# Optimization experiments

Hardware: AMD Instinct MI355X
Metric: run time of the kernel (lower is better)

The kernel has to match this reference:

```python
import jax, jax.numpy as jnp
import numpy as np

DY = jnp.array([-1, -1, -1, 0, 0, 0, 1, 1, 1], dtype=jnp.float32)
DX = jnp.array([-1, 0, 1, -1, 0, 1, -1, 0, 1], dtype=jnp.float32)
REG = jnp.stack([DY, DX])  # (2,9) regular_matrix: row0 = dy, row1 = dx
EPS = 1e-5


def conv3x3(x, w, b):
    y = jax.lax.conv_general_dilated(x, w, (1, 1), ((1, 1), (1, 1)),
                                     dimension_numbers=('NCHW', 'OIHW', 'NCHW'))
    return y + b[None, :, None, None]


def batchnorm(x, gamma, beta):
    m = x.mean((0, 2, 3), keepdims=True)
    v = x.var((0, 2, 3), keepdims=True)
    return gamma[None, :, None, None] * (x - m) * jax.lax.rsqrt(v + EPS) + beta[None, :, None, None]


def make_offset(tm, tr):
    # tm: (N,4,H,W) per-pixel 2x2 matrix, tr: (N,2,H,W) translation
    N, _, H, W = tm.shape
    M = tm.transpose(0, 2, 3, 1).reshape(N, H, W, 2, 2)
    off = jnp.einsum('nhwij,jk->nhwik', M, REG) - REG          # (N,H,W,2,9)
    off = off.transpose(0, 4, 3, 1, 2)                          # (N,9,2,H,W)
    off = off + tr[:, None, :, :, :]                            # broadcast translation over K
    return off


def deform_conv(x, off, w):
    # x: (N,C,H,W), off: (N,9,2,H,W) with [...,0]=dy,[...,1]=dx, w: (Co,C,3,3)
    N, C, H, W = x.shape
    K = 9
    py = jnp.arange(H, dtype=x.dtype)[None, None, :, None] + DY[None, :, None, None] + off[:, :, 0]
    px = jnp.arange(W, dtype=x.dtype)[None, None, None, :] + DX[None, :, None, None] + off[:, :, 1]
    y0 = jnp.floor(py)
    x0 = jnp.floor(px)
    wy = py - y0
    wx = px - x0
    y0i = y0.astype(jnp.int32)
    x0i = x0.astype(jnp.int32)
    x_flat = x.reshape(N, C, H * W)

    def corner(yi, xi, wgt):
        valid = (yi >= 0) & (yi < H) & (xi >= 0) & (xi < W)
        idx = jnp.clip(yi, 0, H - 1) * W + jnp.clip(xi, 0, W - 1)   # (N,K,H,W)
        g = jax.vmap(lambda xf, ix: xf[:, ix])(x_flat, idx.reshape(N, -1))
        g = g.reshape(N, C, K, H, W)
        return g * (wgt * valid)[:, None]

    cols = (corner(y0i, x0i, (1 - wy) * (1 - wx))
            + corner(y0i, x0i + 1, (1 - wy) * wx)
            + corner(y0i + 1, x0i, wy * (1 - wx))
            + corner(y0i + 1, x0i + 1, wy * wx))
    Co = w.shape[0]
    return jnp.einsum('nckhw,ock->nohw', cols, w.reshape(Co, C, K))


def setup_inputs() -> dict:
    key = jax.random.key(0)
    ks = jax.random.split(key, 16)
    N, C, Co, H, W = 4, 256, 256, 64, 64
    s_off = 0.02   # small init so offsets stay near the regular grid
    s_w = 0.05
    return {
        'x': jax.random.normal(ks[0], (N, C, H, W), jnp.float32),
        'tm1_w': jax.random.normal(ks[1], (4, C, 3, 3), jnp.float32) * s_off,
        'tm1_b': jax.random.normal(ks[2], (4,), jnp.float32) * s_off,
        'tr1_w': jax.random.normal(ks[3], (2, C, 3, 3), jnp.float32) * s_off,
        'tr1_b': jax.random.normal(ks[4], (2,), jnp.float32) * s_off,
        'dcn1_w': jax.random.normal(ks[5], (Co, C, 3, 3), jnp.float32) * s_w,
        'bn1_g': jnp.ones((Co,), jnp.float32),
        'bn1_b': jnp.zeros((Co,), jnp.float32),
        'tm2_w': jax.random.normal(ks[6], (4, Co, 3, 3), jnp.float32) * s_off,
        'tm2_b': jax.random.normal(ks[7], (4,), jnp.float32) * s_off,
        'tr2_w': jax.random.normal(ks[8], (2, Co, 3, 3), jnp.float32) * s_off,
        'tr2_b': jax.random.normal(ks[9], (2,), jnp.float32) * s_off,
        'dcn2_w': jax.random.normal(ks[10], (Co, Co, 3, 3), jnp.float32) * s_w,
        'bn2_g': jnp.ones((Co,), jnp.float32),
        'bn2_b': jnp.zeros((Co,), jnp.float32),
    }


def reference(x, tm1_w, tm1_b, tr1_w, tr1_b, dcn1_w, bn1_g, bn1_b,
              tm2_w, tm2_b, tr2_w, tr2_b, dcn2_w, bn2_g, bn2_b):
    residual = x
    off1 = make_offset(conv3x3(x, tm1_w, tm1_b), conv3x3(x, tr1_w, tr1_b))
    out = deform_conv(x, off1, dcn1_w)
    out = jax.nn.relu(batchnorm(out, bn1_g, bn1_b))
    off2 = make_offset(conv3x3(out, tm2_w, tm2_b), conv3x3(out, tr2_w, tr2_b))
    out = deform_conv(out, off2, dcn2_w)
    out = batchnorm(out, bn2_g, bn2_b)
    return jax.nn.relu(out + residual)
```

## Files before the change

### kernel.cpp

```cpp
#include <hip/hip_runtime.h>
#include <hip/hip_bf16.h>

#define HH 64
#define WW 64
#define HWSZ 4096
#define NBATCH 4
#define CCH 256
#define NPIX 16384
#define CK 2304
#define EPSB 1e-5f

typedef __attribute__((ext_vector_type(8))) short bf16x8;
typedef __attribute__((ext_vector_type(4))) float f32x4;

static __device__ __forceinline__ unsigned short f2bf(float f){
  __hip_bfloat16 h = __float2bfloat16(f);
  return *(unsigned short*)&h;
}

#if __has_builtin(__builtin_amdgcn_global_load_lds)
#define GLD(S,D) __builtin_amdgcn_global_load_lds((const __attribute__((address_space(1))) void*)(S), \
                                                  (__attribute__((address_space(3))) void*)(D), 16, 0, 0)
#else
#define GLD(S,D) (*(bf16x8*)((char*)(D) + lane*16) = *(const bf16x8*)(S))
#endif

__global__ __launch_bounds__(256) void k_transpose_in(const float* __restrict__ x,
                                                      float* __restrict__ xT){
  __shared__ float tile[64][65];
  int hw0 = blockIdx.x * 64;
  int c0  = blockIdx.y * 64;
  int n   = blockIdx.z;
  int t = threadIdx.x;
  int col = t & 63, rb = t >> 6;
#pragma unroll
  for (int r = 0; r < 16; ++r){
    int cl = rb + r*4;
    tile[cl][col] = x[(size_t)(n*CCH + c0 + cl)*HWSZ + hw0 + col];
  }
  __syncthreads();
#pragma unroll
  for (int r = 0; r < 16; ++r){
    int hwl = rb + r*4;
    xT[(size_t)(n*HWSZ + hw0 + hwl)*CCH + c0 + col] = tile[col][hwl];
  }
}

__global__ void k_woff_perm(const float* __restrict__ tmw, const float* __restrict__ trw,
                            float* __restrict__ woff){
  int idx = blockIdx.x*256 + threadIdx.x;
  if (idx >= 9*6*CCH) return;
  int k = idx / (6*CCH); int rem = idx % (6*CCH); int j = rem >> 8; int c = rem & 255;
  float v = (j < 4) ? tmw[(size_t)(j*CCH + c)*9 + k]
                    : trw[(size_t)((j-4)*CCH + c)*9 + k];
  woff[idx] = v;
}

__global__ void k_wgemm_perm(const float* __restrict__ w, __hip_bfloat16* __restrict__ wp){
  int idx = blockIdx.x*256 + threadIdx.x;
  if (idx >= CCH*CK) return;
  int blk = idx >> 13;
  int e   = idx & 8191;
  int o   = e >> 5;
  int el  = e & 31;
  int tap = blk >> 3, cb = blk & 7;
  int c   = cb*32 + (el ^ ((o & 3) << 3));
  wp[idx] = __float2bfloat16(w[(size_t)o*CK + c*9 + tap]);
}

__global__ __launch_bounds__(256) void k_offsets(const float* __restrict__ src,
    const float* __restrict__ wofft, const float* __restrict__ tmb,
    const float* __restrict__ trb, float* __restrict__ off){
  int t = threadIdx.x;
  int wid = t >> 6, lane = t & 63;
  int pbase = blockIdx.x*32 + wid*8;
  int n = pbase >> 12; int hw = pbase & 4095; int h = hw >> 6; int w0 = hw & 63;
  const float* base = src + (size_t)n*HWSZ*CCH + lane*4;

  float acc[8][6];
#pragma unroll
  for (int pi = 0; pi < 8; ++pi)
#pragma unroll
    for (int j = 0; j < 6; ++j) acc[pi][j] = 0.f;

  for (int k = 0; k < 9; ++k){
    int ky = k/3 - 1, kx = k%3 - 1;
    int yy = h + ky;
    if (yy < 0 || yy >= HH) continue;
    float4 wv[6];
#pragma unroll
    for (int j = 0; j < 6; ++j)
      wv[j] = *(const float4*)(wofft + ((k*6 + j) << 8) + lane*4);
#pragma unroll
    for (int pi = 0; pi < 8; ++pi){
      int xx = w0 + pi + kx;
      if (xx < 0 || xx >= WW) continue;
      float4 s4 = *(const float4*)(base + (size_t)(yy*WW + xx)*CCH);
#pragma unroll
      for (int j = 0; j < 6; ++j)
        acc[pi][j] += s4.x*wv[j].x + s4.y*wv[j].y + s4.z*wv[j].z + s4.w*wv[j].w;
    }
  }

#pragma unroll
  for (int pi = 0; pi < 8; ++pi)
#pragma unroll
    for (int j = 0; j < 6; ++j){
      float v = acc[pi][j];
#pragma unroll
      for (int m = 32; m >= 1; m >>= 1) v += __shfl_xor(v, m);
      acc[pi][j] = v;
    }

  float b0 = tmb[0], b1 = tmb[1], b2 = tmb[2], b3 = tmb[3];
  float c0 = trb[0], c1 = trb[1];
  if (lane < 18){
    int k = lane >> 1, comp = lane & 1;
    float dy = (float)(k/3 - 1), dx = (float)(k%3 - 1);
#pragma unroll
    for (int pi = 0; pi < 8; ++pi){
      int p = pbase + pi;
      float val;
      if (comp == 0)
        val = (acc[pi][0] + b0)*dy + (acc[pi][1] + b1)*dx - dy + acc[pi][4] + c0;
      else
        val = (acc[pi][2] + b2)*dy + (acc[pi][3] + b3)*dx - dx + acc[pi][5] + c1;
      off[((size_t)p*9 + k)*2 + comp] = val;
    }
  }
}

__global__ __launch_bounds__(512) void k_dcn(const float* __restrict__ src,
    const float* __restrict__ off, const __hip_bfloat16* __restrict__ wp,
    float* __restrict__ gout){
  __shared__ __hip_bfloat16 Al[2*64*32];
  __shared__ __hip_bfloat16 Bl[2*256*32];
  __shared__ __align__(16) int   t_off[576][4];
  __shared__ __align__(16) float t_w[576][4];

  int t = threadIdx.x;
  int bid = blockIdx.x;
  int tile = (bid & 7)*32 + (bid >> 3);
  int pbase = tile * 64;

  for (int s = t; s < 576; s += 512){
    int px = s / 9, k = s - px*9;
    int p = pbase + px;
    int n = p >> 12; int hw = p & 4095; int h = hw >> 6; int w = hw & 63;
    float2 of = *(const float2*)(off + ((size_t)p*9 + k)*2);
    float py = (float)(h + k/3 - 1) + of.x;
    float px_ = (float)(w + (k - (k/3)*3) - 1) + of.y;
    float y0f = floorf(py), x0f = floorf(px_);
    float wy = py - y0f, wx = px_ - x0f;
    int y0 = (int)y0f, x0 = (int)x0f;
    int y1 = y0 + 1, x1 = x0 + 1;
    float w00 = (1.f-wy)*(1.f-wx), w01 = (1.f-wy)*wx;
    float w10 = wy*(1.f-wx),       w11 = wy*wx;
    if (y0 < 0 || y0 >= HH) { w00 = 0.f; w01 = 0.f; }
    if (y1 < 0 || y1 >= HH) { w10 = 0.f; w11 = 0.f; }
    if (x0 < 0 || x0 >= WW) { w00 = 0.f; w10 = 0.f; }
    if (x1 < 0 || x1 >= WW) { w01 = 0.f; w11 = 0.f; }
    int y0c = min(max(y0,0),HH-1), y1c = min(max(y1,0),HH-1);
    int x0c = min(max(x0,0),WW-1), x1c = min(max(x1,0),WW-1);
    int pbix = n << 12;
    t_off[s][0] = (pbix + y0c*WW + x0c) << 10;
    t_off[s][1] = (pbix + y0c*WW + x1c) << 10;
    t_off[s][2] = (pbix + y1c*WW + x0c) << 10;
    t_off[s][3] = (pbix + y1c*WW + x1c) << 10;
    t_w[s][0] = w00; t_w[s][1] = w01; t_w[s][2] = w10; t_w[s][3] = w11;
  }
  __syncthreads();

  int wid = t >> 6, lane = t & 63;
  int pxl = t >> 3, q = t & 7;
  const char* sbase = (const char*)src;
  const char* wpb = (const char*)wp;

  int abyte = pxl*64 + ((q*8) ^ ((pxl & 3) << 4));

  int kq = lane >> 4, fr = lane & 15;
  int abr[4], bbr[2];
#pragma unroll
  for (int mi = 0; mi < 4; ++mi){
    int apx = mi*16 + fr;
    abr[mi] = apx*64 + ((kq*16) ^ ((apx & 3) << 4));
  }
#pragma unroll
  for (int ni = 0; ni < 2; ++ni){
    int o = wid*32 + ni*16 + fr;
    bbr[ni] = o*64 + ((kq*16) ^ ((o & 3) << 4));
  }

  f32x4 acc[4][2];
#pragma unroll
  for (int i = 0; i < 4; ++i)
#pragma unroll
    for (int j = 0; j < 2; ++j)
      acc[i][j] = (f32x4){0.f,0.f,0.f,0.f};

  {
    int slot = pxl*9;
    int chb = q << 4;
    int4 o4 = *(const int4*)t_off[slot];
    float4 wv = *(const float4*)t_w[slot];
    float4 ga = *(const float4*)(sbase + (size_t)(unsigned)(o4.x + chb));
    float4 gb = *(const float4*)(sbase + (size_t)(unsigned)(o4.y + chb));
    float4 gc = *(const float4*)(sbase + (size_t)(unsigned)(o4.z + chb));
    float4 gd = *(const float4*)(sbase + (size_t)(unsigned)(o4.w + chb));
    const char* bsrc = wpb + wid*2048 + lane*16;
    GLD(bsrc,        (char*)Bl + wid*2048);
    GLD(bsrc + 1024, (char*)Bl + wid*2048 + 1024);
    float v0 = wv.x*ga.x + wv.y*gb.x + wv.z*gc.x + wv.w*gd.x;
    float v1 = wv.x*ga.y + wv.y*gb.y + wv.z*gc.y + wv.w*gd.y;
    float v2 = wv.x*ga.z + wv.y*gb.z + wv.z*gc.z + wv.w*gd.z;
    float v3 = wv.x*ga.w + wv.y*gb.w + wv.z*gc.w + wv.w*gd.w;
    ushort4 st; st.x = f2bf(v0); st.y = f2bf(v1); st.z = f2bf(v2); st.w = f2bf(v3);
    *(ushort4*)((char*)Al + abyte) = st;
    __syncthreads();
  }

  for (int kt = 0; kt < 72; ++kt){
    int cur = kt & 1, nxt = cur ^ 1;
    int ktn = (kt < 71) ? kt + 1 : 71;
    int slotn = pxl*9 + (ktn >> 3);
    int chb = ((ktn & 7) << 7) + (q << 4);
    int4 o4 = *(const int4*)t_off[slotn];
    float4 wv = *(const float4*)t_w[slotn];
    float4 ga = *(const float4*)(sbase + (size_t)(unsigned)(o4.x + chb));
    float4 gb = *(const float4*)(sbase + (size_t)(unsigned)(o4.y + chb));
    float4 gc = *(const float4*)(sbase + (size_t)(unsigned)(o4.z + chb));
    float4 gd = *(const float4*)(sbase + (size_t)(unsigned)(o4.w + chb));
    const char* bsrc = wpb + (size_t)ktn*16384 + wid*2048 + lane*16;
    char* bdst = (char*)Bl + nxt*16384 + wid*2048;
    GLD(bsrc,        bdst);
    GLD(bsrc + 1024, bdst + 1024);

    const char* Ac = (const char*)Al + cur*4096;
    const char* Bc = (const char*)Bl + cur*16384;
    bf16x8 av0 = *(const bf16x8*)(Ac + abr[0]);
    bf16x8 av1 = *(const bf16x8*)(Ac + abr[1]);
    bf16x8 av2 = *(const bf16x8*)(Ac + abr[2]);
    bf16x8 av3 = *(const bf16x8*)(Ac + abr[3]);
    bf16x8 bv0 = *(const bf16x8*)(Bc + bbr[0]);
    bf16x8 bv1 = *(const bf16x8*)(Bc + bbr[1]);
    acc[0][0] = __builtin_amdgcn_mfma_f32_16x16x32_bf16(av0, bv0, acc[0][0], 0, 0, 0);
    acc[0][1] = __builtin_amdgcn_mfma_f32_16x16x32_bf16(av0, bv1, acc[0][1], 0, 0, 0);
    acc[1][0] = __builtin_amdgcn_mfma_f32_16x16x32_bf16(av1, bv0, acc[1][0], 0, 0, 0);
    acc[1][1] = __builtin_amdgcn_mfma_f32_16x16x32_bf16(av1, bv1, acc[1][1], 0, 0, 0);
    acc[2][0] = __builtin_amdgcn_mfma_f32_16x16x32_bf16(av2, bv0, acc[2][0], 0, 0, 0);
    acc[2][1] = __builtin_amdgcn_mfma_f32_16x16x32_bf16(av2, bv1, acc[2][1], 0, 0, 0);
    acc[3][0] = __builtin_amdgcn_mfma_f32_16x16x32_bf16(av3, bv0, acc[3][0], 0, 0, 0);
    acc[3][1] = __builtin_amdgcn_mfma_f32_16x16x32_bf16(av3, bv1, acc[3][1], 0, 0, 0);

    float v0 = wv.x*ga.x + wv.y*gb.x + wv.z*gc.x + wv.w*gd.x;
    float v1 = wv.x*ga.y + wv.y*gb.y + wv.z*gc.y + wv.w*gd.y;
    float v2 = wv.x*ga.z + wv.y*gb.z + wv.z*gc.z + wv.w*gd.z;
    float v3 = wv.x*ga.w + wv.y*gb.w + wv.z*gc.w + wv.w*gd.w;
    ushort4 st; st.x = f2bf(v0); st.y = f2bf(v1); st.z = f2bf(v2); st.w = f2bf(v3);
    *(ushort4*)((char*)Al + nxt*4096 + abyte) = st;
    __syncthreads();
  }

#pragma unroll
  for (int mi = 0; mi < 4; ++mi)
#pragma unroll
    for (int ni = 0; ni < 2; ++ni){
      int rr = pbase + mi*16 + (lane>>4)*4;
      int cc = wid*32 + ni*16 + fr;
#pragma unroll
      for (int r = 0; r < 4; ++r)
        gout[(size_t)(rr + r)*CCH + cc] = acc[mi][ni][r];
    }
}

__global__ __launch_bounds__(256) void k_bn_stats(const float* __restrict__ v,
                                                  float* __restrict__ stats){
  int t = threadIdx.x;
  int p0 = blockIdx.x * 128;
  float s = 0.f, ss = 0.f;
  for (int i = 0; i < 128; ++i){
    float x = v[(size_t)(p0 + i)*CCH + t];
    s += x; ss += x*x;
  }
  atomicAdd(&stats[t], s);
  atomicAdd(&stats[CCH + t], ss);
}

__global__ __launch_bounds__(256) void k_bn_apply(const float* __restrict__ v,
    const float* __restrict__ stats, const float* __restrict__ g,
    const float* __restrict__ bb, float* __restrict__ y){
  const float inv = 1.f/16384.f;
  for (size_t i = (size_t)blockIdx.x*256 + threadIdx.x; i < (size_t)NPIX*CCH;
       i += (size_t)gridDim.x*256){
    int c = (int)(i & 255);
    float mean = stats[c]*inv;
    float var  = stats[CCH + c]*inv - mean*mean;
    float sc = g[c]*rsqrtf(var + EPSB);
    float sh = bb[c] - mean*sc;
    float val = fmaf(v[i], sc, sh);
    y[i] = val > 0.f ? val : 0.f;
  }
}

__global__ __launch_bounds__(256) void k_final(const float* __restrict__ v,
    const float* __restrict__ stats, const float* __restrict__ g,
    const float* __restrict__ bb, const float* __restrict__ x,
    float* __restrict__ out){
  __shared__ float tile[64][65];
  int hw0 = blockIdx.x * 64;
  int o0  = blockIdx.y * 64;
  int n   = blockIdx.z;
  int t = threadIdx.x;
  int col = t & 63, rb = t >> 6;
  const float inv = 1.f/16384.f;
#pragma unroll
  for (int r = 0; r < 16; ++r){
    int pl = rb + r*4;
    tile[pl][col] = v[(size_t)(n*HWSZ + hw0 + pl)*CCH + o0 + col];
  }
  __syncthreads();
#pragma unroll
  for (int r = 0; r < 16; ++r){
    int ol = rb + r*4;
    int o = o0 + ol;
    float mean = stats[o]*inv;
    float var  = stats[CCH + o]*inv - mean*mean;
    float sc = g[o]*rsqrtf(var + EPSB);
    float sh = bb[o] - mean*sc;
    size_t gi = (size_t)(n*CCH + o)*HWSZ + hw0 + col;
    float val = fmaf(tile[col][ol], sc, sh) + x[gi];
    out[gi] = val > 0.f ? val : 0.f;
  }
}

extern "C" void kernel_launch(void* const* d_in, const int* in_sizes, int n_in,
                              void* d_out, int out_size, void* d_ws, size_t ws_size,
                              hipStream_t stream){
  const float* x     = (const float*)d_in[0];
  const float* tm1_w = (const float*)d_in[1];
  const float* tm1_b = (const float*)d_in[2];
  const float* tr1_w = (const float*)d_in[3];
  const float* tr1_b = (const float*)d_in[4];
  const float* dcn1_w= (const float*)d_in[5];
  const float* bn1_g = (const float*)d_in[6];
  const float* bn1_b = (const float*)d_in[7];
  const float* tm2_w = (const float*)d_in[8];
  const float* tm2_b = (const float*)d_in[9];
  const float* tr2_w = (const float*)d_in[10];
  const float* tr2_b = (const float*)d_in[11];
  const float* dcn2_w= (const float*)d_in[12];
  const float* bn2_g = (const float*)d_in[13];
  const float* bn2_b = (const float*)d_in[14];
  float* out = (float*)d_out;

  char* ws = (char*)d_ws;
  size_t cursor = 0;
  auto alloc = [&](size_t bytes)->char*{
    char* p = ws + cursor; cursor += (bytes + 255) & ~(size_t)255; return p;
  };
  float* xT    = (float*)alloc((size_t)NPIX*CCH*4);
  float* ybuf  = (float*)alloc((size_t)NPIX*CCH*4);
  float* gout  = (float*)alloc((size_t)NPIX*CCH*4);
  float* offb  = (float*)alloc((size_t)NPIX*9*2*4);
  float* woff1 = (float*)alloc(9*6*CCH*4);
  float* woff2 = (float*)alloc(9*6*CCH*4);
  __hip_bfloat16* wg1 = (__hip_bfloat16*)alloc((size_t)CCH*CK*2);
  __hip_bfloat16* wg2 = (__hip_bfloat16*)alloc((size_t)CCH*CK*2);
  float* stats = (float*)alloc(1024*4);

  hipMemsetAsync(stats, 0, 1024*4, stream);
  k_transpose_in<<<dim3(64,4,4),256,0,stream>>>(x, xT);
  k_woff_perm<<<54,256,0,stream>>>(tm1_w, tr1_w, woff1);
  k_woff_perm<<<54,256,0,stream>>>(tm2_w, tr2_w, woff2);
  k_wgemm_perm<<<2304,256,0,stream>>>(dcn1_w, wg1);
  k_wgemm_perm<<<2304,256,0,stream>>>(dcn2_w, wg2);

  k_offsets<<<512,256,0,stream>>>(xT, woff1, tm1_b, tr1_b, offb);
  k_dcn<<<256,512,0,stream>>>(xT, offb, wg1, gout);
  k_bn_stats<<<128,256,0,stream>>>(gout, stats);
  k_bn_apply<<<2048,256,0,stream>>>(gout, stats, bn1_g, bn1_b, ybuf);

  k_offsets<<<512,256,0,stream>>>(ybuf, woff2, tm2_b, tr2_b, offb);
  k_dcn<<<256,512,0,stream>>>(ybuf, offb, wg2, gout);
  k_bn_stats<<<128,256,0,stream>>>(gout, stats + 512);
  k_final<<<dim3(64,4,4),256,0,stream>>>(gout, stats + 512, bn2_g, bn2_b, x, out);
}
```

Measured before the change: 219.3 us.

## Deepen DCN K-loop pipeline to two stages with 4-buffer B and manual waitcnts

Restructures the deformable-conv GEMM main loop so the bilinear gathers and B-weight global-to-LDS loads are issued two K-steps ahead. The B tile moves to a 4-slot LDS ring and the gathers alternate between two register sets, with the loop unrolled by two. __syncthreads is replaced by explicit vmcnt/lgkmcnt waits and s_barrier, so the gathers can overlap MFMA work. In exchange it uses more registers and 32KB more LDS, which may lower occupancy, and the hand-counted vmcnt(6) is easy to get wrong.

```diff
diff --git a/kernel.cpp b/kernel.cpp
--- a/kernel.cpp
+++ b/kernel.cpp
@@ -130,11 +130,13 @@
   }
 }
 
+struct Gset { float4 a, b, c, d; };
+
 __global__ __launch_bounds__(512) void k_dcn(const float* __restrict__ src,
     const float* __restrict__ off, const __hip_bfloat16* __restrict__ wp,
     float* __restrict__ gout){
   __shared__ __hip_bfloat16 Al[2*64*32];
-  __shared__ __hip_bfloat16 Bl[2*256*32];
+  __shared__ __hip_bfloat16 Bl[4*256*32];
   __shared__ __align__(16) int   t_off[576][4];
   __shared__ __align__(16) float t_w[576][4];
 
@@ -179,16 +181,14 @@
   int abyte = pxl*64 + ((q*8) ^ ((pxl & 3) << 4));
 
   int kq = lane >> 4, fr = lane & 15;
-  int abr[4], bbr[2];
-#pragma unroll
-  for (int mi = 0; mi < 4; ++mi){
-    int apx = mi*16 + fr;
-    abr[mi] = apx*64 + ((kq*16) ^ ((apx & 3) << 4));
-  }
-#pragma unroll
-  for (int ni = 0; ni < 2; ++ni){
-    int o = wid*32 + ni*16 + fr;
-    bbr[ni] = o*64 + ((kq*16) ^ ((o & 3) << 4));
+  int abr0, abr1, abr2, abr3, bbr0, bbr1;
+  {
+    int apx0 = 0*16 + fr;  abr0 = apx0*64 + ((kq*16) ^ ((apx0 & 3) << 4));
+    int apx1 = 1*16 + fr;  abr1 = apx1*64 + ((kq*16) ^ ((apx1 & 3) << 4));
+    int apx2 = 2*16 + fr;  abr2 = apx2*64 + ((kq*16) ^ ((apx2 & 3) << 4));
+    int apx3 = 3*16 + fr;  abr3 = apx3*64 + ((kq*16) ^ ((apx3 & 3) << 4));
+    int o0 = wid*32 + 0*16 + fr;  bbr0 = o0*64 + ((kq*16) ^ ((o0 & 3) << 4));
+    int o1 = wid*32 + 1*16 + fr;  bbr1 = o1*64 + ((kq*16) ^ ((o1 & 3) << 4));
   }
 
   f32x4 acc[4][2];
@@ -198,51 +198,57 @@
     for (int j = 0; j < 2; ++j)
       acc[i][j] = (f32x4){0.f,0.f,0.f,0.f};
 
-  {
-    int slot = pxl*9;
-    int chb = q << 4;
+  Gset gA, gB;
+
+  auto issue_gather = [&](int ktn, Gset& g){
+    int slot = pxl*9 + (ktn >> 3);
+    int chb = ((ktn & 7) << 7) + (q << 4);
     int4 o4 = *(const int4*)t_off[slot];
+    g.a = *(const float4*)(sbase + (size_t)(unsigned)(o4.x + chb));
+    g.b = *(const float4*)(sbase + (size_t)(unsigned)(o4.y + chb));
+    g.c = *(const float4*)(sbase + (size_t)(unsigned)(o4.z + chb));
+    g.d = *(const float4*)(sbase + (size_t)(unsigned)(o4.w + chb));
+  };
+  auto convert_write = [&](int ktc, Gset& g){
+    int slot = pxl*9 + (ktc >> 3);
     float4 wv = *(const float4*)t_w[slot];
-    float4 ga = *(const float4*)(sbase + (size_t)(unsigned)(o4.x + chb));
-    float4 gb = *(const float4*)(sbase + (size_t)(unsigned)(o4.y + chb));
-    float4 gc = *(const float4*)(sbase + (size_t)(unsigned)(o4.z + chb));
-    float4 gd = *(const float4*)(sbase + (size_t)(unsigned)(o4.w + chb));
-    const char* bsrc = wpb + wid*2048 + lane*16;
-    GLD(bsrc,        (char*)Bl + wid*2048);
-    GLD(bsrc + 1024, (char*)Bl + wid*2048 + 1024);
-    float v0 = wv.x*ga.x + wv.y*gb.x + wv.z*gc.x + wv.w*gd.x;
-    float v1 = wv.x*ga.y + wv.y*gb.y + wv.z*gc.y + wv.w*gd.y;
-    float v2 = wv.x*ga.z + wv.y*gb.z + wv.z*gc.z + wv.w*gd.z;
-    float v3 = wv.x*ga.w + wv.y*gb.w + wv.z*gc.w + wv.w*gd.w;
+    float v0 = wv.x*g.a.x + wv.y*g.b.x + wv.z*g.c.x + wv.w*g.d.x;
+    float v1 = wv.x*g.a.y + wv.y*g.b.y + wv.z*g.c.y + wv.w*g.d.y;
+    float v2 = wv.x*g.a.z + wv.y*g.b.z + wv.z*g.c.z + wv.w*g.d.z;
+    float v3 = wv.x*g.a.w + wv.y*g.b.w + wv.z*g.c.w + wv.w*g.d.w;
     ushort4 st; st.x = f2bf(v0); st.y = f2bf(v1); st.z = f2bf(v2); st.w = f2bf(v3);
-    *(ushort4*)((char*)Al + abyte) = st;
-    __syncthreads();
-  }
-
-  for (int kt = 0; kt < 72; ++kt){
-    int cur = kt & 1, nxt = cur ^ 1;
-    int ktn = (kt < 71) ? kt + 1 : 71;
-    int slotn = pxl*9 + (ktn >> 3);
-    int chb = ((ktn & 7) << 7) + (q << 4);
-    int4 o4 = *(const int4*)t_off[slotn];
-    float4 wv = *(const float4*)t_w[slotn];
-    float4 ga = *(const float4*)(sbase + (size_t)(unsigned)(o4.x + chb));
-    float4 gb = *(const float4*)(sbase + (size_t)(unsigned)(o4.y + chb));
-    float4 gc = *(const float4*)(sbase + (size_t)(unsigned)(o4.z + chb));
-    float4 gd = *(const float4*)(sbase + (size_t)(unsigned)(o4.w + chb));
-    const char* bsrc = wpb + (size_t)ktn*16384 + wid*2048 + lane*16;
-    char* bdst = (char*)Bl + nxt*16384 + wid*2048;
+    *(ushort4*)((char*)Al + (ktc & 1)*4096 + abyte) = st;
+  };
+  auto issue_B = [&](int ktb){
+    const char* bsrc = wpb + (size_t)ktb*16384 + wid*2048 + lane*16;
+    char* bdst = (char*)Bl + (ktb & 3)*16384 + wid*2048;
     GLD(bsrc,        bdst);
     GLD(bsrc + 1024, bdst + 1024);
-
-    const char* Ac = (const char*)Al + cur*4096;
-    const char* Bc = (const char*)Bl + cur*16384;
-    bf16x8 av0 = *(const bf16x8*)(Ac + abr[0]);
-    bf16x8 av1 = *(const bf16x8*)(Ac + abr[1]);
-    bf16x8 av2 = *(const bf16x8*)(Ac + abr[2]);
-    bf16x8 av3 = *(const bf16x8*)(Ac + abr[3]);
-    bf16x8 bv0 = *(const bf16x8*)(Bc + bbr[0]);
-    bf16x8 bv1 = *(const bf16x8*)(Bc + bbr[1]);
+  };
+
+  issue_B(0);
+  issue_B(1);
+  asm volatile("" ::: "memory");
+  issue_gather(0, gA);
+  issue_gather(1, gB);
+  convert_write(0, gA);
+  asm volatile("s_waitcnt lgkmcnt(0)" ::: "memory");
+  __builtin_amdgcn_s_barrier();
+
+  auto body = [&](int kt, Gset& gIss, Gset& gCnv){
+    asm volatile("s_waitcnt vmcnt(6)" ::: "memory");
+    __builtin_amdgcn_sched_barrier(0);
+    const char* Ac = (const char*)Al + (kt & 1)*4096;
+    const char* Bc = (const char*)Bl + (kt & 3)*16384;
+    bf16x8 av0 = *(const bf16x8*)(Ac + abr0);
+    bf16x8 av1 = *(const bf16x8*)(Ac + abr1);
+    bf16x8 av2 = *(const bf16x8*)(Ac + abr2);
+    bf16x8 av3 = *(const bf16x8*)(Ac + abr3);
+    bf16x8 bv0 = *(const bf16x8*)(Bc + bbr0);
+    bf16x8 bv1 = *(const bf16x8*)(Bc + bbr1);
+    if (kt <= 69) issue_B(kt + 2);
+    asm volatile("" ::: "memory");
+    if (kt <= 69) issue_gather(kt + 2, gIss);
     acc[0][0] = __builtin_amdgcn_mfma_f32_16x16x32_bf16(av0, bv0, acc[0][0], 0, 0, 0);
     acc[0][1] = __builtin_amdgcn_mfma_f32_16x16x32_bf16(av0, bv1, acc[0][1], 0, 0, 0);
     acc[1][0] = __builtin_amdgcn_mfma_f32_16x16x32_bf16(av1, bv0, acc[1][0], 0, 0, 0);
@@ -251,14 +257,14 @@
     acc[2][1] = __builtin_amdgcn_mfma_f32_16x16x32_bf16(av2, bv1, acc[2][1], 0, 0, 0);
     acc[3][0] = __builtin_amdgcn_mfma_f32_16x16x32_bf16(av3, bv0, acc[3][0], 0, 0, 0);
     acc[3][1] = __builtin_amdgcn_mfma_f32_16x16x32_bf16(av3, bv1, acc[3][1], 0, 0, 0);
-
-    float v0 = wv.x*ga.x + wv.y*gb.x + wv.z*gc.x + wv.w*gd.x;
-    float v1 = wv.x*ga.y + wv.y*gb.y + wv.z*gc.y + wv.w*gd.y;
-    float v2 = wv.x*ga.z + wv.y*gb.z + wv.z*gc.z + wv.w*gd.z;
-    float v3 = wv.x*ga.w + wv.y*gb.w + wv.z*gc.w + wv.w*gd.w;
-    ushort4 st; st.x = f2bf(v0); st.y = f2bf(v1); st.z = f2bf(v2); st.w = f2bf(v3);
-    *(ushort4*)((char*)Al + nxt*4096 + abyte) = st;
-    __syncthreads();
+    if (kt <= 70) convert_write(kt + 1, gCnv);
+    asm volatile("s_waitcnt lgkmcnt(0)" ::: "memory");
+    __builtin_amdgcn_s_barrier();
+  };
+
+  for (int kk = 0; kk < 72; kk += 2){
+    body(kk + 0, gA, gB);
+    body(kk + 1, gB, gA);
   }
 
 #pragma unroll
```

After: 206.1 us. 1.06x faster.
